# Kernel optimization log

Measured on AMD Instinct MI355X. Metric: run time of the kernel, lower is better.

## Reference

```python
import jax, jax.numpy as jnp
import numpy as np

# conv hyperparams matching init_kwargs (kernel=3, stride=1, pad=1, dilation=1, dg=1)
KH = KW = 3
SH = SW = 1
PH = PW = 1
DH = DW = 1


def setup_inputs() -> dict:
    key = jax.random.key(0)
    k1, k2, k3 = jax.random.split(key, 3)
    N, C, H, W = 4, 64, 128, 128
    OC, KN = 64, KH * KW
    x = jax.random.normal(k1, (N, C, H, W), jnp.float32)
    # offset channels: deformable_groups * kernel_n * 2, ordered (y, x) per point
    offset = jax.random.normal(k2, (N, KN * 2, H, W), jnp.float32)
    weight = jax.random.normal(k3, (OC, C, KN), jnp.float32) * 0.05
    return {"x": x, "offset": offset, "weight": weight}


def _bilinear(img, ix, iy):
    # img: (C, H, W); ix, iy: (KN, OH, OW) pixel coords; align_corners=True, zeros padding
    H, W = img.shape[1], img.shape[2]
    x0 = jnp.floor(ix)
    y0 = jnp.floor(iy)
    x1 = x0 + 1.0
    y1 = y0 + 1.0
    wx1 = ix - x0
    wx0 = 1.0 - wx1
    wy1 = iy - y0
    wy0 = 1.0 - wy1

    def gather(xc, yc, w):
        xi = jnp.clip(xc, 0, W - 1).astype(jnp.int32)
        yi = jnp.clip(yc, 0, H - 1).astype(jnp.int32)
        m = ((xc >= 0) & (xc <= W - 1) & (yc >= 0) & (yc <= H - 1)).astype(img.dtype)
        return img[:, yi, xi] * (w * m)[None]  # (C, KN, OH, OW)

    return (gather(x0, y0, wx0 * wy0) + gather(x1, y0, wx1 * wy0)
            + gather(x0, y1, wx0 * wy1) + gather(x1, y1, wx1 * wy1))


def reference(x, offset, weight):
    N, C, H, W = x.shape
    KN = weight.shape[2]
    OH, OW = offset.shape[2], offset.shape[3]
    half_h = (H - 1) / 2.0
    half_w = (W - 1) / 2.0
    # base mesh in normalized [-1,1] coords (same for every kernel point, per source)
    ys = jnp.arange(OH, dtype=x.dtype) * SH - PH + ((KH - 1) // 2) * DH
    xs = jnp.arange(OW, dtype=x.dtype) * SW - PW + ((KW - 1) // 2) * DW
    base_gy = (ys - half_h) / half_h  # (OH,)
    base_gx = (xs - half_w) / half_w  # (OW,)
    off = offset.reshape(N, KN, 2, OH, OW)
    gy = base_gy[None, None, :, None] + off[:, :, 0] / half_h  # (N, KN, OH, OW)
    gx = base_gx[None, None, None, :] + off[:, :, 1] / half_w
    # back to pixel coords (align_corners=True)
    ix = (gx + 1.0) * half_w
    iy = (gy + 1.0) * half_h
    sampled = jax.vmap(_bilinear)(x, ix, iy)  # (N, C, KN, OH, OW)
    # weight (OC, C, KN) contracted over (C, KN); note: source forward never adds bias
    out = jnp.einsum('oik,nikhw->nohw', weight, sampled)
    return out
```

## Files before the change

kernel.cpp:

```cpp
#include <hip/hip_runtime.h>


#define NB 4
#define CI 64
#define HH 128
#define WW 128
#define OCH 64
#define KNN 9
#define HW (HH * WW)

typedef unsigned int u32;
typedef unsigned short u16;
typedef __attribute__((ext_vector_type(8))) short bf16x8;
typedef __attribute__((ext_vector_type(4))) float f32x4;

__device__ inline u16 f2bf(float f) {
    u32 u = __float_as_uint(f);
    return (u16)((u + 0x7fffu + ((u >> 16) & 1u)) >> 16);
}
__device__ inline u32 pk2(float lo, float hi) {
    return (u32)f2bf(lo) | ((u32)f2bf(hi) << 16);
}
__device__ inline void up2(u32 u, float& lo, float& hi) {
    lo = __uint_as_float(u << 16);
    hi = __uint_as_float(u & 0xffff0000u);
}

__global__ __launch_bounds__(256) void prep_kernel(const float* __restrict__ x,
                                                   const float* __restrict__ w,
                                                   u16* __restrict__ xT,
                                                   u16* __restrict__ wf) {
    __shared__ float T[64 * 68];
    const int tid = threadIdx.x;
    if (blockIdx.x < NB * 256) {
        const int n = blockIdx.x >> 8;
        const int hw0 = (blockIdx.x & 255) << 6;
#pragma unroll
        for (int jj = 0; jj < 4; jj++) {
            int c = (tid >> 4) + (jj << 4);
            int hwq = (tid & 15) << 2;
            float4 v = *(const float4*)&x[(((n << 6) + c) << 14) + hw0 + hwq];
            *(float4*)&T[c * 68 + hwq] = v;
        }
        __syncthreads();
        const int hw_l = tid >> 2;
        const int cb = (tid & 3) << 4;
        u32 ou[8];
#pragma unroll
        for (int k = 0; k < 8; k++) {
            ou[k] = pk2(T[(cb + 2 * k) * 68 + hw_l], T[(cb + 2 * k + 1) * 68 + hw_l]);
        }
        u16* dst = xT + ((size_t)((n << 14) + hw0 + hw_l) << 6) + cb;
        *(uint4*)dst = make_uint4(ou[0], ou[1], ou[2], ou[3]);
        *(uint4*)(dst + 8) = make_uint4(ou[4], ou[5], ou[6], ou[7]);
    } else {
        int i = (blockIdx.x - NB * 256) * 256 + tid;
        if (i < KNN * 2 * 4 * 64 * 8) {
            int j = i & 7, l = (i >> 3) & 63, strip = (i >> 9) & 3,
                chunk = (i >> 11) & 1, kn = i >> 12;
            int oc = strip * 16 + (l & 15);
            int c = chunk * 32 + ((l >> 4) & 3) * 8 + j;
            wf[i] = f2bf(w[(oc * CI + c) * KNN + kn]);
        }
    }
}

__global__ __launch_bounds__(256, 4) void dcn_main_kernel(const u16* __restrict__ xT,
                                                          const float* __restrict__ off,
                                                          const u16* __restrict__ wf,
                                                          float* __restrict__ out) {
    const int tid = threadIdx.x;
    const int l = tid & 63;
    const int wv = tid >> 6;
    const int gw = (blockIdx.x << 2) + wv;
    const int p0 = gw << 4;
    const int n = p0 >> 14;
    const int rr0 = p0 & 16383;
    const int col = l & 15;
    const int rr = rr0 + col;
    const int oh = rr >> 7, ow = rr & 127;
    const int cbase = (l >> 4) << 3;
    const u16* xTn = xT + ((size_t)n << 20);
    const float* offn = off + n * (2 * KNN * HW);
    const bf16x8* wfv = (const bf16x8*)wf;

    f32x4 acc[4] = {{0, 0, 0, 0}, {0, 0, 0, 0}, {0, 0, 0, 0}, {0, 0, 0, 0}};

    for (int kn = 0; kn < KNN; kn++) {
        float offy = offn[(2 * kn) * HW + rr];
        float offx = offn[(2 * kn + 1) * HW + rr];
        float iy = (float)oh + offy, ix = (float)ow + offx;
        float y0f = floorf(iy), x0f = floorf(ix);
        float wy1 = iy - y0f, wy0 = 1.f - wy1;
        float wx1 = ix - x0f, wx0 = 1.f - wx1;
        float my0 = (y0f >= 0.f && y0f <= 127.f) ? 1.f : 0.f;
        float my1 = (y0f >= -1.f && y0f <= 126.f) ? 1.f : 0.f;
        float mx0 = (x0f >= 0.f && x0f <= 127.f) ? 1.f : 0.f;
        float mx1 = (x0f >= -1.f && x0f <= 126.f) ? 1.f : 0.f;
        float w00 = wy0 * wx0 * my0 * mx0, w01 = wy0 * wx1 * my0 * mx1;
        float w10 = wy1 * wx0 * my1 * mx0, w11 = wy1 * wx1 * my1 * mx1;
        int y0 = min(max((int)y0f, 0), 127), y1 = min(max((int)y0f + 1, 0), 127);
        int x0 = min(max((int)x0f, 0), 127), x1 = min(max((int)x0f + 1, 0), 127);
        const u16* b00 = xTn + (((y0 << 7) + x0) << 6);
        const u16* b01 = xTn + (((y0 << 7) + x1) << 6);
        const u16* b10 = xTn + (((y1 << 7) + x0) << 6);
        const u16* b11 = xTn + (((y1 << 7) + x1) << 6);
#pragma unroll
        for (int ch = 0; ch < 2; ch++) {
            const int c = (ch << 5) + cbase;
            uint4 q00 = *(const uint4*)(b00 + c);
            uint4 q01 = *(const uint4*)(b01 + c);
            uint4 q10 = *(const uint4*)(b10 + c);
            uint4 q11 = *(const uint4*)(b11 + c);
            const u32* a00 = (const u32*)&q00;
            const u32* a01 = (const u32*)&q01;
            const u32* a10 = (const u32*)&q10;
            const u32* a11 = (const u32*)&q11;
            union { u32 u[4]; bf16x8 v; } B;
#pragma unroll
            for (int k = 0; k < 4; k++) {
                float p0l, p0h, p1l, p1h, p2l, p2h, p3l, p3h;
                up2(a00[k], p0l, p0h);
                up2(a01[k], p1l, p1h);
                up2(a10[k], p2l, p2h);
                up2(a11[k], p3l, p3h);
                float slo = p0l * w00 + p1l * w01 + p2l * w10 + p3l * w11;
                float shi = p0h * w00 + p1h * w01 + p2h * w10 + p3h * w11;
                B.u[k] = pk2(slo, shi);
            }
#pragma unroll
            for (int s = 0; s < 4; s++) {
                bf16x8 A = wfv[(((kn << 1) + ch) << 2 | s) * 64 + l];
                acc[s] = __builtin_amdgcn_mfma_f32_16x16x32_bf16(A, B.v, acc[s], 0, 0, 0);
            }
        }
    }
    const int rq = l >> 4;
    float* op = out + ((size_t)(n * OCH) << 14);
#pragma unroll
    for (int s = 0; s < 4; s++) {
        const int ocb = (s << 4) + (rq << 2);
#pragma unroll
        for (int g = 0; g < 4; g++) {
            op[((ocb + g) << 14) + rr] = acc[s][g];
        }
    }
}

__global__ __launch_bounds__(256) void dcn_fallback_kernel(
    const float* __restrict__ x, const float* __restrict__ off,
    const float* __restrict__ w, float* __restrict__ out) {
    int p = blockIdx.x * blockDim.x + threadIdx.x;
    int n = p / HW, r = p % HW, oh = r / WW, ow = r % WW;
    float acc[OCH];
#pragma unroll
    for (int i = 0; i < OCH; i++) acc[i] = 0.f;
    const float* xn = x + n * (CI * HW);
    const float* offn = off + n * (2 * KNN * HW);
    for (int kn = 0; kn < KNN; kn++) {
        float iy = (float)oh + offn[(2 * kn) * HW + r];
        float ix = (float)ow + offn[(2 * kn + 1) * HW + r];
        float y0f = floorf(iy), x0f = floorf(ix);
        float wy1 = iy - y0f, wy0 = 1.f - wy1, wx1 = ix - x0f, wx0 = 1.f - wx1;
        float my0 = (y0f >= 0.f && y0f <= 127.f) ? 1.f : 0.f;
        float my1 = (y0f >= -1.f && y0f <= 126.f) ? 1.f : 0.f;
        float mx0 = (x0f >= 0.f && x0f <= 127.f) ? 1.f : 0.f;
        float mx1 = (x0f >= -1.f && x0f <= 126.f) ? 1.f : 0.f;
        float w00 = wy0 * wx0 * my0 * mx0, w01 = wy0 * wx1 * my0 * mx1;
        float w10 = wy1 * wx0 * my1 * mx0, w11 = wy1 * wx1 * my1 * mx1;
        int y0 = min(max((int)y0f, 0), 127), y1 = min(max((int)y0f + 1, 0), 127);
        int x0 = min(max((int)x0f, 0), 127), x1 = min(max((int)x0f + 1, 0), 127);
        int o00 = y0 * WW + x0, o01 = y0 * WW + x1, o10 = y1 * WW + x0, o11 = y1 * WW + x1;
        for (int c = 0; c < CI; c++) {
            const float* xc = xn + c * HW;
            float s = xc[o00] * w00 + xc[o01] * w01 + xc[o10] * w10 + xc[o11] * w11;
#pragma unroll
            for (int oc = 0; oc < OCH; oc++) acc[oc] += w[(oc * CI + c) * KNN + kn] * s;
        }
    }
    float* outp = out + n * (OCH * HW) + r;
#pragma unroll
    for (int oc = 0; oc < OCH; oc++) outp[oc * HW] = acc[oc];
}

extern "C" void kernel_launch(void* const* d_in, const int* in_sizes, int n_in,
                              void* d_out, int out_size, void* d_ws, size_t ws_size,
                              hipStream_t stream) {
    const float* x = (const float*)d_in[0];
    const float* off = (const float*)d_in[1];
    const float* w = (const float*)d_in[2];
    float* out = (float*)d_out;

    const size_t xT_elems = (size_t)NB * HW * CI;
    const size_t wf_elems = (size_t)KNN * 2 * 4 * 64 * 8;
    const size_t need = (xT_elems + wf_elems) * sizeof(u16);

    if (ws_size >= need) {
        u16* xT = (u16*)d_ws;
        u16* wfr = xT + xT_elems;
        const int wf_blocks = (int)((wf_elems + 255) / 256);
        prep_kernel<<<NB * 256 + wf_blocks, 256, 0, stream>>>(x, w, xT, wfr);
        dcn_main_kernel<<<1024, 256, 0, stream>>>(xT, off, wfr, out);
    } else {
        dcn_fallback_kernel<<<(NB * HW) / 256, 256, 0, stream>>>(x, off, w, out);
    }
}
```

Measured before the change: 116.0 us.

## Software-pipeline deformable gathers and stage weights in LDS via async loads

Restructures the main loop so each kernel point's corner gathers and bilinear coordinates are issued one iteration ahead and held in double-buffered registers. Weight fragments are staged into a double-buffered LDS tile with global_load_lds, replacing per-lane global loads, and all offsets are preloaded up front. This is meant to hide gather latency behind MFMA and interpolation work. In exchange it raises register pressure (occupancy hint lowered from 4 to 3), adds a block barrier per kernel point, and swaps the manual bf16 pack for the library round-to-nearest conversion.

New measurement: 110.8 us. 1.05x faster.

```diff
diff --git a/kernel.cpp b/kernel.cpp
--- a/kernel.cpp
+++ b/kernel.cpp
@@ -1,4 +1,5 @@
 #include <hip/hip_runtime.h>
+#include <hip/hip_bf16.h>
 
 
 #define NB 4
@@ -14,6 +15,9 @@
 typedef __attribute__((ext_vector_type(8))) short bf16x8;
 typedef __attribute__((ext_vector_type(4))) float f32x4;
 
+typedef const __attribute__((address_space(1))) u32* gas_ptr;
+typedef __attribute__((address_space(3))) u32* las_ptr;
+
 __device__ inline u16 f2bf(float f) {
     u32 u = __float_as_uint(f);
     return (u16)((u + 0x7fffu + ((u >> 16) & 1u)) >> 16);
@@ -24,6 +28,15 @@
 __device__ inline void up2(u32 u, float& lo, float& hi) {
     lo = __uint_as_float(u << 16);
     hi = __uint_as_float(u & 0xffff0000u);
+}
+__device__ inline u32 pkrn(float lo, float hi) {
+    __hip_bfloat162 h = __float22bfloat162_rn(float2{lo, hi});
+    union { __hip_bfloat162 b; u32 u; } c;
+    c.b = h;
+    return c.u;
+}
+__device__ inline void gload_lds16(const u16* g, u16* s) {
+    __builtin_amdgcn_global_load_lds((gas_ptr)g, (las_ptr)s, 16, 0, 0);
 }
 
 __global__ __launch_bounds__(256) void prep_kernel(const float* __restrict__ x,
@@ -65,10 +78,11 @@
     }
 }
 
-__global__ __launch_bounds__(256, 4) void dcn_main_kernel(const u16* __restrict__ xT,
+__global__ __launch_bounds__(256, 3) void dcn_main_kernel(const u16* __restrict__ xT,
                                                           const float* __restrict__ off,
                                                           const u16* __restrict__ wf,
                                                           float* __restrict__ out) {
+    __shared__ __align__(16) u16 Abuf[2][4096];
     const int tid = threadIdx.x;
     const int l = tid & 63;
     const int wv = tid >> 6;
@@ -82,14 +96,24 @@
     const int cbase = (l >> 4) << 3;
     const u16* xTn = xT + ((size_t)n << 20);
     const float* offn = off + n * (2 * KNN * HW);
-    const bf16x8* wfv = (const bf16x8*)wf;
+
+    float offy[KNN], offx[KNN];
+#pragma unroll
+    for (int kn = 0; kn < KNN; kn++) {
+        offy[kn] = offn[(2 * kn) * HW + rr];
+        offx[kn] = offn[(2 * kn + 1) * HW + rr];
+    }
 
     f32x4 acc[4] = {{0, 0, 0, 0}, {0, 0, 0, 0}, {0, 0, 0, 0}, {0, 0, 0, 0}};
 
-    for (int kn = 0; kn < KNN; kn++) {
-        float offy = offn[(2 * kn) * HW + rr];
-        float offx = offn[(2 * kn + 1) * HW + rr];
-        float iy = (float)oh + offy, ix = (float)ow + offx;
+    float W[2][4];
+    int O[2][4];
+    uint4 G0[2][4];
+    uint4 G1[2][4];
+
+    auto calc = [&](int kn) {
+        const int p = kn & 1;
+        float iy = (float)oh + offy[kn], ix = (float)ow + offx[kn];
         float y0f = floorf(iy), x0f = floorf(ix);
         float wy1 = iy - y0f, wy0 = 1.f - wy1;
         float wx1 = ix - x0f, wx0 = 1.f - wx1;
@@ -97,44 +121,82 @@
         float my1 = (y0f >= -1.f && y0f <= 126.f) ? 1.f : 0.f;
         float mx0 = (x0f >= 0.f && x0f <= 127.f) ? 1.f : 0.f;
         float mx1 = (x0f >= -1.f && x0f <= 126.f) ? 1.f : 0.f;
-        float w00 = wy0 * wx0 * my0 * mx0, w01 = wy0 * wx1 * my0 * mx1;
-        float w10 = wy1 * wx0 * my1 * mx0, w11 = wy1 * wx1 * my1 * mx1;
+        W[p][0] = wy0 * wx0 * my0 * mx0;
+        W[p][1] = wy0 * wx1 * my0 * mx1;
+        W[p][2] = wy1 * wx0 * my1 * mx0;
+        W[p][3] = wy1 * wx1 * my1 * mx1;
         int y0 = min(max((int)y0f, 0), 127), y1 = min(max((int)y0f + 1, 0), 127);
         int x0 = min(max((int)x0f, 0), 127), x1 = min(max((int)x0f + 1, 0), 127);
-        const u16* b00 = xTn + (((y0 << 7) + x0) << 6);
-        const u16* b01 = xTn + (((y0 << 7) + x1) << 6);
-        const u16* b10 = xTn + (((y1 << 7) + x0) << 6);
-        const u16* b11 = xTn + (((y1 << 7) + x1) << 6);
-#pragma unroll
-        for (int ch = 0; ch < 2; ch++) {
-            const int c = (ch << 5) + cbase;
-            uint4 q00 = *(const uint4*)(b00 + c);
-            uint4 q01 = *(const uint4*)(b01 + c);
-            uint4 q10 = *(const uint4*)(b10 + c);
-            uint4 q11 = *(const uint4*)(b11 + c);
-            const u32* a00 = (const u32*)&q00;
-            const u32* a01 = (const u32*)&q01;
-            const u32* a10 = (const u32*)&q10;
-            const u32* a11 = (const u32*)&q11;
-            union { u32 u[4]; bf16x8 v; } B;
-#pragma unroll
-            for (int k = 0; k < 4; k++) {
-                float p0l, p0h, p1l, p1h, p2l, p2h, p3l, p3h;
-                up2(a00[k], p0l, p0h);
-                up2(a01[k], p1l, p1h);
-                up2(a10[k], p2l, p2h);
-                up2(a11[k], p3l, p3h);
-                float slo = p0l * w00 + p1l * w01 + p2l * w10 + p3l * w11;
-                float shi = p0h * w00 + p1h * w01 + p2h * w10 + p3h * w11;
-                B.u[k] = pk2(slo, shi);
-            }
-#pragma unroll
-            for (int s = 0; s < 4; s++) {
-                bf16x8 A = wfv[(((kn << 1) + ch) << 2 | s) * 64 + l];
-                acc[s] = __builtin_amdgcn_mfma_f32_16x16x32_bf16(A, B.v, acc[s], 0, 0, 0);
-            }
-        }
-    }
+        O[p][0] = ((y0 << 7) + x0) << 6;
+        O[p][1] = ((y0 << 7) + x1) << 6;
+        O[p][2] = ((y1 << 7) + x0) << 6;
+        O[p][3] = ((y1 << 7) + x1) << 6;
+    };
+    auto gather = [&](int kn, int ch, uint4* G) {
+        const int p = kn & 1;
+        const int c = (ch << 5) + cbase;
+#pragma unroll
+        for (int k = 0; k < 4; k++) G[k] = *(const uint4*)(xTn + O[p][k] + c);
+    };
+    auto stageA = [&](int kn) {
+        const int b = kn & 1;
+        const u16* g = wf + kn * 4096 + wv * 1024 + l * 8;
+        u16* s = &Abuf[b][wv * 1024 + l * 8];
+        gload_lds16(g, s);
+        gload_lds16(g + 512, s + 512);
+    };
+    auto interp = [&](int kn, const uint4* G, bf16x8& Bv) {
+        const int p = kn & 1;
+        const u32* a0 = (const u32*)&G[0];
+        const u32* a1 = (const u32*)&G[1];
+        const u32* a2 = (const u32*)&G[2];
+        const u32* a3 = (const u32*)&G[3];
+        union { u32 u[4]; bf16x8 v; } B;
+#pragma unroll
+        for (int k = 0; k < 4; k++) {
+            float p0l, p0h, p1l, p1h, p2l, p2h, p3l, p3h;
+            up2(a0[k], p0l, p0h);
+            up2(a1[k], p1l, p1h);
+            up2(a2[k], p2l, p2h);
+            up2(a3[k], p3l, p3h);
+            float slo = p0l * W[p][0] + p1l * W[p][1] + p2l * W[p][2] + p3l * W[p][3];
+            float shi = p0h * W[p][0] + p1h * W[p][1] + p2h * W[p][2] + p3h * W[p][3];
+            B.u[k] = pkrn(slo, shi);
+        }
+        Bv = B.v;
+    };
+    auto mfma_ch = [&](int kn, int ch, bf16x8 Bv) {
+        const int b = kn & 1;
+#pragma unroll
+        for (int s4 = 0; s4 < 4; s4++) {
+            bf16x8 A = *(const bf16x8*)&Abuf[b][(((ch << 2) + s4) * 64 + l) * 8];
+            acc[s4] = __builtin_amdgcn_mfma_f32_16x16x32_bf16(A, Bv, acc[s4], 0, 0, 0);
+        }
+    };
+
+    calc(0);
+    stageA(0);
+    gather(0, 0, G0[0]);
+    gather(0, 1, G1[0]);
+    __syncthreads();
+
+#pragma unroll
+    for (int kn = 0; kn < KNN; kn++) {
+        if (kn + 1 < KNN) {
+            calc(kn + 1);
+            stageA(kn + 1);
+            gather(kn + 1, 0, G0[(kn + 1) & 1]);
+        }
+        bf16x8 B0;
+        interp(kn, G0[kn & 1], B0);
+        if (kn + 1 < KNN) gather(kn + 1, 1, G1[(kn + 1) & 1]);
+        mfma_ch(kn, 0, B0);
+        bf16x8 B1;
+        interp(kn, G1[kn & 1], B1);
+        mfma_ch(kn, 1, B1);
+        __syncthreads();
+    }
+
     const int rq = l >> 4;
     float* op = out + ((size_t)(n * OCH) << 14);
 #pragma unroll
```

## Stage weights in LDS, tile pixels as 2D patches, preload offsets

Applied to the files above, without the earlier changes.

Each block now copies the full bf16 weight fragment set (72 KB) into LDS with global_load_lds and reads the MFMA A operands from LDS rather than from global memory. Pixels are remapped from 16-pixel row strips to 8x8 spatial patches, with each wave covering a 4x4 sub-tile, so the bilinear gathers of neighbouring pixels hit more of the same cache lines. All nine offset pairs are loaded up front and the kn loop is fully unrolled. The 72 KB of LDS per block and the launch bound lowered from 4 to 2 reduce occupancy, and storing the output from 4-wide rows gives less coalesced writes.

New measurement: 114.5 us. Within noise of the previous version (-1.3%).

```diff
diff --git a/kernel.cpp b/kernel.cpp
--- a/kernel.cpp
+++ b/kernel.cpp
@@ -1,4 +1,5 @@
 #include <hip/hip_runtime.h>
+#include <hip/hip_bf16.h>
 
 
 #define NB 4
@@ -14,6 +15,9 @@
 typedef __attribute__((ext_vector_type(8))) short bf16x8;
 typedef __attribute__((ext_vector_type(4))) float f32x4;
 
+typedef const __attribute__((address_space(1))) u32* gas_ptr;
+typedef __attribute__((address_space(3))) u32* las_ptr;
+
 __device__ inline u16 f2bf(float f) {
     u32 u = __float_as_uint(f);
     return (u16)((u + 0x7fffu + ((u >> 16) & 1u)) >> 16);
@@ -24,6 +28,9 @@
 __device__ inline void up2(u32 u, float& lo, float& hi) {
     lo = __uint_as_float(u << 16);
     hi = __uint_as_float(u & 0xffff0000u);
+}
+__device__ inline void gload_lds16(const u16* g, u16* s) {
+    __builtin_amdgcn_global_load_lds((gas_ptr)g, (las_ptr)s, 16, 0, 0);
 }
 
 __global__ __launch_bounds__(256) void prep_kernel(const float* __restrict__ x,
@@ -65,31 +72,50 @@
     }
 }
 
-__global__ __launch_bounds__(256, 4) void dcn_main_kernel(const u16* __restrict__ xT,
+__global__ __launch_bounds__(256, 2) void dcn_main_kernel(const u16* __restrict__ xT,
                                                           const float* __restrict__ off,
                                                           const u16* __restrict__ wf,
                                                           float* __restrict__ out) {
+    __shared__ __align__(16) u16 Abuf[KNN * 4096];
     const int tid = threadIdx.x;
     const int l = tid & 63;
     const int wv = tid >> 6;
-    const int gw = (blockIdx.x << 2) + wv;
-    const int p0 = gw << 4;
-    const int n = p0 >> 14;
-    const int rr0 = p0 & 16383;
+
+    {
+        const u16* g = wf + tid * 8;
+        u16* s = Abuf + tid * 8;
+#pragma unroll
+        for (int i = 0; i < 18; i++) {
+            gload_lds16(g + i * 2048, s + i * 2048);
+        }
+    }
+
+    const int n = blockIdx.x >> 8;
+    const int patch = blockIdx.x & 255;
+    const int py = ((patch >> 4) << 3), px = ((patch & 15) << 3);
+    const int qy = ((wv >> 1) << 2), qx = ((wv & 1) << 2);
     const int col = l & 15;
-    const int rr = rr0 + col;
-    const int oh = rr >> 7, ow = rr & 127;
+    const int oh = py + qy + (col >> 2);
+    const int ow = px + qx + (col & 3);
+    const int rr = (oh << 7) + ow;
     const int cbase = (l >> 4) << 3;
     const u16* xTn = xT + ((size_t)n << 20);
     const float* offn = off + n * (2 * KNN * HW);
-    const bf16x8* wfv = (const bf16x8*)wf;
+
+    float offy[KNN], offx[KNN];
+#pragma unroll
+    for (int kn = 0; kn < KNN; kn++) {
+        offy[kn] = offn[(2 * kn) * HW + rr];
+        offx[kn] = offn[(2 * kn + 1) * HW + rr];
+    }
+
+    __syncthreads();
 
     f32x4 acc[4] = {{0, 0, 0, 0}, {0, 0, 0, 0}, {0, 0, 0, 0}, {0, 0, 0, 0}};
 
+#pragma unroll
     for (int kn = 0; kn < KNN; kn++) {
-        float offy = offn[(2 * kn) * HW + rr];
-        float offx = offn[(2 * kn + 1) * HW + rr];
-        float iy = (float)oh + offy, ix = (float)ow + offx;
+        float iy = (float)oh + offy[kn], ix = (float)ow + offx[kn];
         float y0f = floorf(iy), x0f = floorf(ix);
         float wy1 = iy - y0f, wy0 = 1.f - wy1;
         float wx1 = ix - x0f, wx0 = 1.f - wx1;
@@ -97,44 +123,44 @@
         float my1 = (y0f >= -1.f && y0f <= 126.f) ? 1.f : 0.f;
         float mx0 = (x0f >= 0.f && x0f <= 127.f) ? 1.f : 0.f;
         float mx1 = (x0f >= -1.f && x0f <= 126.f) ? 1.f : 0.f;
-        float w00 = wy0 * wx0 * my0 * mx0, w01 = wy0 * wx1 * my0 * mx1;
-        float w10 = wy1 * wx0 * my1 * mx0, w11 = wy1 * wx1 * my1 * mx1;
+        float W0 = wy0 * wx0 * my0 * mx0, W1 = wy0 * wx1 * my0 * mx1;
+        float W2 = wy1 * wx0 * my1 * mx0, W3 = wy1 * wx1 * my1 * mx1;
         int y0 = min(max((int)y0f, 0), 127), y1 = min(max((int)y0f + 1, 0), 127);
         int x0 = min(max((int)x0f, 0), 127), x1 = min(max((int)x0f + 1, 0), 127);
-        const u16* b00 = xTn + (((y0 << 7) + x0) << 6);
-        const u16* b01 = xTn + (((y0 << 7) + x1) << 6);
-        const u16* b10 = xTn + (((y1 << 7) + x0) << 6);
-        const u16* b11 = xTn + (((y1 << 7) + x1) << 6);
+        int O0 = ((y0 << 7) + x0) << 6, O1 = ((y0 << 7) + x1) << 6;
+        int O2 = ((y1 << 7) + x0) << 6, O3 = ((y1 << 7) + x1) << 6;
+
 #pragma unroll
         for (int ch = 0; ch < 2; ch++) {
             const int c = (ch << 5) + cbase;
-            uint4 q00 = *(const uint4*)(b00 + c);
-            uint4 q01 = *(const uint4*)(b01 + c);
-            uint4 q10 = *(const uint4*)(b10 + c);
-            uint4 q11 = *(const uint4*)(b11 + c);
-            const u32* a00 = (const u32*)&q00;
-            const u32* a01 = (const u32*)&q01;
-            const u32* a10 = (const u32*)&q10;
-            const u32* a11 = (const u32*)&q11;
+            uint4 q0 = *(const uint4*)(xTn + O0 + c);
+            uint4 q1 = *(const uint4*)(xTn + O1 + c);
+            uint4 q2 = *(const uint4*)(xTn + O2 + c);
+            uint4 q3 = *(const uint4*)(xTn + O3 + c);
+            const u32* a0 = (const u32*)&q0;
+            const u32* a1 = (const u32*)&q1;
+            const u32* a2 = (const u32*)&q2;
+            const u32* a3 = (const u32*)&q3;
             union { u32 u[4]; bf16x8 v; } B;
 #pragma unroll
             for (int k = 0; k < 4; k++) {
                 float p0l, p0h, p1l, p1h, p2l, p2h, p3l, p3h;
-                up2(a00[k], p0l, p0h);
-                up2(a01[k], p1l, p1h);
-                up2(a10[k], p2l, p2h);
-                up2(a11[k], p3l, p3h);
-                float slo = p0l * w00 + p1l * w01 + p2l * w10 + p3l * w11;
-                float shi = p0h * w00 + p1h * w01 + p2h * w10 + p3h * w11;
+                up2(a0[k], p0l, p0h);
+                up2(a1[k], p1l, p1h);
+                up2(a2[k], p2l, p2h);
+                up2(a3[k], p3l, p3h);
+                float slo = p0l * W0 + p1l * W1 + p2l * W2 + p3l * W3;
+                float shi = p0h * W0 + p1h * W1 + p2h * W2 + p3h * W3;
                 B.u[k] = pk2(slo, shi);
             }
 #pragma unroll
             for (int s = 0; s < 4; s++) {
-                bf16x8 A = wfv[(((kn << 1) + ch) << 2 | s) * 64 + l];
+                bf16x8 A = *(const bf16x8*)&Abuf[(((kn << 1) + ch) << 2 | s) * 512 + l * 8];
                 acc[s] = __builtin_amdgcn_mfma_f32_16x16x32_bf16(A, B.v, acc[s], 0, 0, 0);
             }
         }
     }
+
     const int rq = l >> 4;
     float* op = out + ((size_t)(n * OCH) << 14);
 #pragma unroll
@@ -200,7 +226,7 @@
         u16* wfr = xT + xT_elems;
         const int wf_blocks = (int)((wf_elems + 255) / 256);
         prep_kernel<<<NB * 256 + wf_blocks, 256, 0, stream>>>(x, w, xT, wfr);
-        dcn_main_kernel<<<1024, 256, 0, stream>>>(xT, off, wfr, out);
+        dcn_main_kernel<<<NB * 256, 256, 0, stream>>>(xT, off, wfr, out);
     } else {
         dcn_fallback_kernel<<<(NB * HW) / 256, 256, 0, stream>>>(x, off, w, out);
     }
```
